# Optimization experiments

Hardware: AMD Instinct MI355X
Metric: run time of the kernel (lower is better)

## Reference

```python
import jax, jax.numpy as jnp
import numpy as np

NHEAD = 8
EPS = 1e-5


def ln(x, g, b):
    m = x.mean(-1, keepdims=True)
    v = ((x - m) ** 2).mean(-1, keepdims=True)
    return (x - m) * jax.lax.rsqrt(v + EPS) * g + b


def mha_rel(q_in, kv_in, pos_enc, pos_idx, Wqkv, bqkv, Wo, bo):
    # q_in, kv_in: [W, N, C] where N = hn*bs
    w, n, c = q_in.shape
    hd = c // NHEAD
    Wq, Wk, Wv = Wqkv[:c], Wqkv[c:2 * c], Wqkv[2 * c:]
    bq, bk, bv = bqkv[:c], bqkv[c:2 * c], bqkv[2 * c:]
    q = q_in @ Wq.T + bq
    k = kv_in @ Wk.T + bk
    v = kv_in @ Wv.T + bv
    # relative position lookup: [2W-1,1,C] gathered by flat [W*W] -> [W,W,C]
    pe = pos_enc[pos_idx].reshape(w, w, c)
    q_r = pe @ Wq.T + bq
    k_r = pe @ Wk.T + bk
    scale = hd ** -0.5
    q = (q * scale).reshape(w, n, NHEAD, hd)
    q_r = (q_r * scale).reshape(w, w, NHEAD, hd)
    k = k.reshape(w, n, NHEAD, hd)
    v = v.reshape(w, n, NHEAD, hd)
    k_r = k_r.reshape(w, w, NHEAD, hd)
    # content-content + content-pos + pos-content scores: [N, E, W, W']
    attn = (jnp.einsum('wnec,vnec->newv', q, k)
            + jnp.einsum('wnec,wvec->newv', q, k_r)
            + jnp.einsum('vnec,wvec->newv', k, q_r))
    raw = attn
    a = jax.nn.softmax(attn, axis=-1)
    vo = jnp.einsum('newv,vnec->wnec', a, v).reshape(w, n, c)
    vo = vo @ Wo.T + bo
    return vo, raw.sum(axis=1)  # [W,N,C], [N,W,W]


def setup_inputs() -> dict:
    key = jax.random.key(0)
    bs, c, hn, w = 2, 128, 64, 256
    ks = jax.random.split(key, 5)
    feat_left = jax.random.normal(ks[0], (bs, c, hn, w), jnp.float32)
    feat_right = jax.random.normal(ks[1], (bs, c, hn, w), jnp.float32)
    pos = jax.random.normal(ks[2], (2 * w - 1, 1, c), jnp.float32)
    r = jnp.arange(w)
    pos_indexes = (r[:, None] - r[None, :] + w - 1).reshape(-1).astype(jnp.int32)
    Wqkv = jax.random.normal(ks[3], (3 * c, c), jnp.float32) * 0.02
    bqkv = jnp.zeros((3 * c,), jnp.float32)
    Wo = jax.random.normal(ks[4], (c, c), jnp.float32) * 0.02
    bo = jnp.zeros((c,), jnp.float32)
    g1 = jnp.ones((c,), jnp.float32)
    b1 = jnp.zeros((c,), jnp.float32)
    g2 = jnp.ones((c,), jnp.float32)
    b2 = jnp.zeros((c,), jnp.float32)
    return dict(feat_left=feat_left, feat_right=feat_right, pos=pos,
                pos_indexes=pos_indexes, Wqkv=Wqkv, bqkv=bqkv, Wo=Wo, bo=bo,
                g1=g1, b1=b1, g2=g2, b2=b2)


def reference(feat_left, feat_right, pos, pos_indexes, Wqkv, bqkv, Wo, bo, g1, b1, g2, b2):
    bs, c, hn, w = feat_left.shape

    def to_seq(f):  # [bs,c,hn,w] -> [w, hn*bs, c]
        return jnp.transpose(f, (1, 3, 2, 0)).reshape(c, w, hn * bs).transpose(1, 2, 0)

    fl = to_seq(feat_left)
    fr = to_seq(feat_right)
    fl2 = ln(fl, g1, b1)
    fr2 = ln(fr, g1, b1)
    # right attends to left with flipped relative pos enc
    upd_r, _ = mha_rel(fr2, fl2, jnp.flip(pos, axis=0), pos_indexes, Wqkv, bqkv, Wo, bo)
    fr = fr + upd_r
    # left attends to updated right (last_layer=False -> no causal mask)
    fr2 = ln(fr, g2, b2)
    upd_l, raw = mha_rel(fl2, fr2, pos, pos_indexes, Wqkv, bqkv, Wo, bo)
    fl = fl + upd_l
    raw_attn = raw.reshape(hn, bs, w, w).transpose(1, 0, 2, 3)  # [bs,hn,w,w]

    def from_seq(f):  # [w, hn*bs, c] -> [bs,c,hn,w]
        return f.reshape(w, hn, bs, c).transpose(2, 3, 1, 0)

    return from_seq(fl), from_seq(fr), raw_attn
```

## Files before the change

### kernel.cpp

```cpp
#include <hip/hip_runtime.h>
#include <cstddef>

static constexpr int Wd  = 256;
static constexpr int NBd = 128;
static constexpr int Cd  = 128;
static constexpr int BSd = 2;
static constexpr int HNd = 64;
static constexpr size_t SEQF = (size_t)Wd * NBd * Cd;

typedef __attribute__((ext_vector_type(8))) short bf16x8;
typedef __attribute__((ext_vector_type(4))) short bf16x4;
typedef __attribute__((ext_vector_type(4))) float f32x4;
typedef __attribute__((ext_vector_type(2))) float f32x2;

__device__ inline short f2bf(float f) {
  union { float f; unsigned u; } v; v.f = f;
  return (short)((v.u + 0x7FFFu + ((v.u >> 16) & 1u)) >> 16);
}

__global__ __launch_bounds__(256) void k_to_seq_ln(
    const float* __restrict__ fA, const float* __restrict__ fB,
    float* __restrict__ seqA, float* __restrict__ seqB,
    short* __restrict__ lnA, short* __restrict__ lnB,
    const float* __restrict__ g, const float* __restrict__ bb) {
  __shared__ float red[2][8][33];
  __shared__ float mv[2][32];
  const int z = blockIdx.y;
  const float* feat = (z < 128) ? fA : fB;
  float* seq = (z < 128) ? seqA : seqB;
  short* lno = (z < 128) ? lnA : lnB;
  const int hb = z & 127;
  const int h = hb >> 1, b = hb & 1;
  const int n = h * BSd + b;
  const int w0 = blockIdx.x * 32;
  const int t = threadIdx.x;
  const int wl = t & 31, cg = t >> 5, c0 = cg * 16;
  float v[16];
  float s1 = 0.f, s2 = 0.f;
#pragma unroll
  for (int r = 0; r < 16; ++r) {
    v[r] = feat[(((size_t)b * Cd + c0 + r) * HNd + h) * Wd + w0 + wl];
    s1 += v[r]; s2 += v[r] * v[r];
  }
  red[0][cg][wl] = s1; red[1][cg][wl] = s2;
  __syncthreads();
  if (t < 32) {
    float a1 = 0.f, a2 = 0.f;
#pragma unroll
    for (int k = 0; k < 8; ++k) { a1 += red[0][k][t]; a2 += red[1][k][t]; }
    float mean = a1 * (1.0f / Cd);
    float var = a2 * (1.0f / Cd) - mean * mean;
    mv[0][t] = mean; mv[1][t] = rsqrtf(var + 1e-5f);
  }
  __syncthreads();
  const float mean = mv[0][wl], rstd = mv[1][wl];
  float* so = &seq[((size_t)(w0 + wl) * NBd + n) * Cd + c0];
  short* bo_ = &lno[((size_t)(w0 + wl) * NBd + n) * Cd + c0];
#pragma unroll
  for (int r = 0; r < 16; ++r) so[r] = v[r];
#pragma unroll
  for (int r = 0; r < 16; ++r)
    bo_[r] = f2bf((v[r] - mean) * rstd * g[c0 + r] + bb[c0 + r]);
}

__global__ __launch_bounds__(256) void k_from_seq2(const float* __restrict__ seqA,
                                                   const float* __restrict__ seqB,
                                                   float* __restrict__ featA,
                                                   float* __restrict__ featB) {
  __shared__ float tile[32][33];
  int wi0 = blockIdx.x * 32, ci0 = blockIdx.y * 32;
  int z = blockIdx.z;
  const float* seq = (z < 128) ? seqA : seqB;
  float* feat = (z < 128) ? featA : featB;
  int hb = z & 127;
  int h = hb >> 1, b = hb & 1;
  int n = h * BSd + b;
  int tx = threadIdx.x, ty = threadIdx.y;
#pragma unroll
  for (int r = 0; r < 4; ++r) {
    int wi = wi0 + ty + r * 8;
    tile[ty + r * 8][tx] = seq[((size_t)wi * NBd + n) * Cd + ci0 + tx];
  }
  __syncthreads();
#pragma unroll
  for (int r = 0; r < 4; ++r) {
    int ci = ci0 + ty + r * 8;
    feat[(((size_t)b * Cd + ci) * HNd + h) * Wd + wi0 + tx] = tile[tx][ty + r * 8];
  }
}

__global__ __launch_bounds__(256) void k_cvt(const float* __restrict__ w1, short* d1,
                                             const float* __restrict__ w2, short* d2,
                                             const float* __restrict__ w3, short* d3)
{
  int i = blockIdx.x * 256 + threadIdx.x;
  if (i < 49152) d1[i] = f2bf(w1[i]);
  if (i < 16384) d2[i] = f2bf(w2[i]);
  if (i < 65408) d3[i] = f2bf(w3[i]);
}

__global__ __launch_bounds__(256) void k_gemm_bf(
    const short* __restrict__ A, const short* __restrict__ Wt,
    const float* __restrict__ bias, float* __restrict__ outF,
    short* __restrict__ outB, int M, int ldout, int scaleN0, float scale,
    const short* __restrict__ A2, short* __restrict__ outB2, int ldout2, int yCut) {
  const int t = threadIdx.x;
  const int lane = t & 63, wv = t >> 6;
  const int ml = lane & 15, quad = lane >> 4;
  const int m0 = blockIdx.x * 64;
  int yb = blockIdx.y;
  const short* Ap = A;
  short* oB = outB;
  float* oF = outF;
  int ld = ldout;
  int nblk = yb;
  if (yb >= yCut) { Ap = A2; oB = outB2; oF = nullptr; ld = ldout2; nblk = 0; }
  const int n0 = nblk * 128 + wv * 32;
  const bf16x8 zero8 = {0, 0, 0, 0, 0, 0, 0, 0};

  bf16x8 Bfr[2][4];
#pragma unroll
  for (int nf = 0; nf < 2; ++nf)
#pragma unroll
    for (int ks = 0; ks < 4; ++ks)
      Bfr[nf][ks] = *(const bf16x8*)&Wt[(size_t)(n0 + nf * 16 + ml) * 128 + ks * 32 + quad * 8];

  f32x4 acc[4][2];
#pragma unroll
  for (int mf = 0; mf < 4; ++mf)
#pragma unroll
    for (int nf = 0; nf < 2; ++nf) acc[mf][nf] = {0.f, 0.f, 0.f, 0.f};

#pragma unroll
  for (int ks = 0; ks < 4; ++ks) {
    bf16x8 Af[4];
#pragma unroll
    for (int mf = 0; mf < 4; ++mf) {
      int m = m0 + mf * 16 + ml;
      Af[mf] = (m < M) ? *(const bf16x8*)&Ap[(size_t)m * 128 + ks * 32 + quad * 8] : zero8;
    }
#pragma unroll
    for (int mf = 0; mf < 4; ++mf)
#pragma unroll
      for (int nf = 0; nf < 2; ++nf)
        acc[mf][nf] = __builtin_amdgcn_mfma_f32_16x16x32_bf16(Af[mf], Bfr[nf][ks], acc[mf][nf], 0, 0, 0);
  }

#pragma unroll
  for (int nf = 0; nf < 2; ++nf) {
    int n = n0 + nf * 16 + ml;
    float bi = bias[n];
    float sc = (n < scaleN0) ? scale : 1.0f;
#pragma unroll
    for (int mf = 0; mf < 4; ++mf) {
#pragma unroll
      for (int r = 0; r < 4; ++r) {
        int m = m0 + mf * 16 + quad * 4 + r;
        if (m >= M) continue;
        float v = (acc[mf][nf][r] + bi) * sc;
        if (oF) oF[(size_t)m * ld + n] = v;
        if (oB) oB[(size_t)m * ld + n] = f2bf(v);
      }
    }
  }
}

__global__ __launch_bounds__(256) void k_gemm_wo_ln(
    const short* __restrict__ A, const short* __restrict__ Wt,
    const float* __restrict__ bias, const float* __restrict__ res,
    float* __restrict__ outF, short* __restrict__ outLN,
    const float* __restrict__ lng, const float* __restrict__ lnb) {
  const int t = threadIdx.x;
  const int lane = t & 63, wv = t >> 6;
  const int ml = lane & 15, quad = lane >> 4;
  const int m0 = blockIdx.x * 64 + wv * 16;
  const int ii = m0 >> 7;
  const int nn = (m0 & 127) + ml;

  f32x4 acc[8];
#pragma unroll
  for (int nf = 0; nf < 8; ++nf) acc[nf] = {0.f, 0.f, 0.f, 0.f};
#pragma unroll
  for (int ks = 0; ks < 4; ++ks) {
    bf16x8 Af = *(const bf16x8*)&A[(((size_t)nn * 8 + ks * 2 + (quad >> 1)) * 256 + ii) * 16 +
                                   (quad & 1) * 8];
#pragma unroll
    for (int nf = 0; nf < 8; ++nf) {
      bf16x8 Bf = *(const bf16x8*)&Wt[(size_t)(nf * 16 + ml) * 128 + ks * 32 + quad * 8];
      acc[nf] = __builtin_amdgcn_mfma_f32_16x16x32_bf16(Af, Bf, acc[nf], 0, 0, 0);
    }
  }
  float val[8][4];
#pragma unroll
  for (int nf = 0; nf < 8; ++nf) {
    float bi = bias[nf * 16 + ml];
#pragma unroll
    for (int r = 0; r < 4; ++r) {
      int m = m0 + quad * 4 + r;
      val[nf][r] = acc[nf][r] + bi + res[(size_t)m * 128 + nf * 16 + ml];
      outF[(size_t)m * 128 + nf * 16 + ml] = val[nf][r];
    }
  }
  if (outLN) {
#pragma unroll
    for (int r = 0; r < 4; ++r) {
      float s1 = 0.f, s2 = 0.f;
#pragma unroll
      for (int nf = 0; nf < 8; ++nf) { s1 += val[nf][r]; s2 += val[nf][r] * val[nf][r]; }
#pragma unroll
      for (int mk = 1; mk < 16; mk <<= 1) { s1 += __shfl_xor(s1, mk); s2 += __shfl_xor(s2, mk); }
      float mean = s1 * (1.0f / 128.f);
      float var = s2 * (1.0f / 128.f) - mean * mean;
      float rstd = rsqrtf(var + 1e-5f);
      int m = m0 + quad * 4 + r;
#pragma unroll
      for (int nf = 0; nf < 8; ++nf) {
        int nn2 = nf * 16 + ml;
        outLN[(size_t)m * 128 + nn2] = f2bf((val[nf][r] - mean) * rstd * lng[nn2] + lnb[nn2]);
      }
    }
  }
}

template <int PASS>
__global__ __launch_bounds__(256, 4) void k_attn_mfma(
    const short* __restrict__ Qg, int ldq,
    const short* __restrict__ Kg, const short* __restrict__ Vg, int ldkv,
    const short* __restrict__ PP, short* __restrict__ OT) {
  __shared__ short Ks[256][16];
  __shared__ short VTs[16][264];
  __shared__ float R2T[4][2][16][20];
  __shared__ float R3T[4][32][22];

  const int t = threadIdx.x;
  const int n = blockIdx.x;
  const int e = blockIdx.y;
  const int lane = t & 63, wv = t >> 6;
  const int ml = lane & 15, quad = lane >> 4;
  const bool lo = lane < 32;
  const bf16x8 zero8 = {0, 0, 0, 0, 0, 0, 0, 0};
  const f32x4 z4 = {0.f, 0.f, 0.f, 0.f};

#pragma unroll
  for (int it = 0; it < 4; ++it) {
    int idx = t + it * 256;
    int r = idx >> 2, c4 = idx & 3;
    *(bf16x4*)&Ks[r][c4 * 4] =
        *(const bf16x4*)&Kg[((size_t)r * NBd + n) * ldkv + e * 16 + c4 * 4];
  }
#pragma unroll
  for (int it = 0; it < 4; ++it) {
    bf16x4 vv = *(const bf16x4*)&Vg[((size_t)t * NBd + n) * ldkv + e * 16 + it * 4];
    VTs[it * 4 + 0][t] = vv[0];
    VTs[it * 4 + 1][t] = vv[1];
    VTs[it * 4 + 2][t] = vv[2];
    VTs[it * 4 + 3][t] = vv[3];
  }
  __syncthreads();

  const short* PPe = PP + e * 16;
  short* OTb = OT + (size_t)(n * 8 + e) * 256 * 16;

  for (int ip = 0; ip < 4; ++ip) {
    const int i0p = ip * 64;
    const int wb = (PASS == 2) ? i0p : (192 - i0p);
    bf16x8 bQ = lo ? *(const bf16x8*)&Qg[((size_t)(i0p + 16 * wv + ml) * NBd + n) * ldq +
                                         e * 16 + quad * 8]
                   : zero8;
    f32x4 Ot = {0.f, 0.f, 0.f, 0.f};
    float den = 0.f;

    bf16x8 fPQprev;
    {
      int pp = (PASS == 2) ? (wb + 16 * wv + 256 + ml) : (wb - 16 * wv + 48 + ml);
      if (pp > 510) pp = 510;
      const short* pr = &PPe[(size_t)pp * 256];
      bf16x8 fPK0 = lo ? *(const bf16x8*)&pr[128 + quad * 8] : zero8;
      fPQprev     = lo ? *(const bf16x8*)&pr[quad * 8] : zero8;
      f32x4 R2i = __builtin_amdgcn_mfma_f32_16x16x32_bf16(bQ, fPK0, z4, 0, 0, 0);
      *(f32x4*)&R2T[wv][1][ml][quad * 4] = R2i;
    }
    bf16x8 fPK, fPQf;
    {
      int pf = (PASS == 2) ? (wb + 16 * wv + 240 + ml) : (wb - 16 * wv + 64 + ml);
      if (pf > 510) pf = 510;
      const short* prf = &PPe[(size_t)pf * 256];
      fPK  = lo ? *(const bf16x8*)&prf[128 + quad * 8] : zero8;
      fPQf = lo ? *(const bf16x8*)&prf[quad * 8] : zero8;
    }

    unsigned pA0 = 0, pA1 = 0;
#pragma unroll
    for (int jt = 0; jt < 16; ++jt) {
      const int j0 = jt * 16;
      bf16x8 aK = lo ? *(const bf16x8*)&Ks[j0 + ml][quad * 8] : zero8;

      bf16x8 nPK = zero8, nPQ = zero8;
      if (jt < 15) {
        int pf = (PASS == 2) ? (wb + 16 * wv - (j0 + 16) + 240 + ml)
                             : (wb - 16 * wv + (j0 + 16) + 64 + ml);
        if (pf > 510) pf = 510;
        const short* prf = &PPe[(size_t)pf * 256];
        nPK = lo ? *(const bf16x8*)&prf[128 + quad * 8] : zero8;
        nPQ = lo ? *(const bf16x8*)&prf[quad * 8] : zero8;
      }

      f32x4 St  = __builtin_amdgcn_mfma_f32_16x16x32_bf16(aK, bQ, z4, 0, 0, 0);
      f32x4 R2f = __builtin_amdgcn_mfma_f32_16x16x32_bf16(bQ, fPK, z4, 0, 0, 0);
      f32x4 R3a_, R3b_;
      if (PASS == 2) {
        R3a_ = __builtin_amdgcn_mfma_f32_16x16x32_bf16(aK, fPQf, z4, 0, 0, 0);
        R3b_ = __builtin_amdgcn_mfma_f32_16x16x32_bf16(aK, fPQprev, z4, 0, 0, 0);
      } else {
        R3b_ = __builtin_amdgcn_mfma_f32_16x16x32_bf16(aK, fPQf, z4, 0, 0, 0);
        R3a_ = __builtin_amdgcn_mfma_f32_16x16x32_bf16(aK, fPQprev, z4, 0, 0, 0);
      }
      fPQprev = fPQf;
      fPK = nPK;
      fPQf = nPQ;

      *(f32x4*)&R2T[wv][jt & 1][ml][quad * 4] = R2f;
      *(f32x2*)&R3T[wv][ml][quad * 4]          = (f32x2){R3a_[0], R3a_[1]};
      *(f32x2*)&R3T[wv][ml][quad * 4 + 2]      = (f32x2){R3a_[2], R3a_[3]};
      *(f32x2*)&R3T[wv][ml + 16][quad * 4]     = (f32x2){R3b_[0], R3b_[1]};
      *(f32x2*)&R3T[wv][ml + 16][quad * 4 + 2] = (f32x2){R3b_[2], R3b_[3]};

      float pe4[4];
#pragma unroll
      for (int r = 0; r < 4; ++r) {
        const int jl = quad * 4 + r;
        const int pcol = (PASS == 2) ? (ml - jl + 15) : (jl - ml + 15);
        const int hi = pcol >> 4, col = pcol & 15;
        const int bk = (jt & 1) ^ hi ^ (PASS == 1 ? 1 : 0);
        float s = St[r] + R2T[wv][bk][col][ml] + R3T[wv][pcol][jl];
        pe4[r] = __expf(s);
        den += pe4[r];
      }
      unsigned d0, d1;
      asm("v_cvt_pk_bf16_f32 %0, %1, %2" : "=v"(d0) : "v"(pe4[0]), "v"(pe4[1]));
      asm("v_cvt_pk_bf16_f32 %0, %1, %2" : "=v"(d1) : "v"(pe4[2]), "v"(pe4[3]));
      if ((jt & 1) == 0) {
        pA0 = d0;
        pA1 = d1;
      } else {
        unsigned b0 = pA0, b2 = d0, b1 = pA1, b3 = d1;
        asm("v_permlane32_swap_b32 %0, %1" : "+v"(b0), "+v"(b2));
        asm("v_permlane16_swap_b32 %0, %1" : "+v"(b0), "+v"(b2));
        asm("v_permlane32_swap_b32 %0, %1" : "+v"(b1), "+v"(b3));
        asm("v_permlane16_swap_b32 %0, %1" : "+v"(b1), "+v"(b3));
        union { unsigned u[4]; bf16x8 v8; } bp;
        bp.u[0] = b0; bp.u[1] = b1; bp.u[2] = b2; bp.u[3] = b3;
        bf16x8 aVT = *(const bf16x8*)&VTs[ml][(jt >> 1) * 32 + quad * 8];
        Ot = __builtin_amdgcn_mfma_f32_16x16x32_bf16(aVT, bp.v8, Ot, 0, 0, 0);
      }
    }
    den += __shfl_xor(den, 16);
    den += __shfl_xor(den, 32);
    float inv = 1.f / den;
    bf16x4 ob;
    ob[0] = f2bf(Ot[0] * inv); ob[1] = f2bf(Ot[1] * inv);
    ob[2] = f2bf(Ot[2] * inv); ob[3] = f2bf(Ot[3] * inv);
    *(bf16x4*)&OTb[(size_t)(i0p + 16 * wv + ml) * 16 + quad * 4] = ob;
  }
}

__global__ __launch_bounds__(256, 4) void k_raw(
    const short* __restrict__ Qf, const short* __restrict__ Kf,
    const short* __restrict__ PP, float* __restrict__ raw) {
  __shared__ float R2s[4][2][16][17];
  __shared__ float R3s[4][16][34];
  const int t = threadIdx.x;
  const int n = blockIdx.y;
  const int lane = t & 63, wv = t >> 6;
  const int ml = lane & 15, quad = lane >> 4;
  const int it0 = blockIdx.x * 64 + wv * 16;
  const int jt0 = blockIdx.z * 4;
  const f32x4 z4 = {0.f, 0.f, 0.f, 0.f};

  bf16x8 aQ[4];
#pragma unroll
  for (int kc = 0; kc < 4; ++kc)
    aQ[kc] = *(const bf16x8*)&Qf[((size_t)(it0 + ml) * NBd + n) * 384 + kc * 32 + quad * 8];

  float* rbase = &raw[(((size_t)(n & 1) * HNd + (n >> 1)) * Wd + it0) * Wd];

  bf16x8 fPQprev[4];
  {
    int pp = it0 - jt0 * 16 + 256 + ml;
    if (pp > 510) pp = 510;
    const short* pr = &PP[(size_t)pp * 256];
    f32x4 R2i = z4;
#pragma unroll
    for (int kc = 0; kc < 4; ++kc) {
      bf16x8 fPK = *(const bf16x8*)&pr[128 + kc * 32 + quad * 8];
      R2i = __builtin_amdgcn_mfma_f32_16x16x32_bf16(aQ[kc], fPK, R2i, 0, 0, 0);
      fPQprev[kc] = *(const bf16x8*)&pr[kc * 32 + quad * 8];
    }
#pragma unroll
    for (int r = 0; r < 4; ++r) R2s[wv][1][quad * 4 + r][ml] = R2i[r];
  }

#pragma unroll
  for (int jq = 0; jq < 4; ++jq) {
    const int j0 = (jt0 + jq) * 16;
    bf16x8 aK[4];
#pragma unroll
    for (int kc = 0; kc < 4; ++kc)
      aK[kc] = *(const bf16x8*)&Kf[((size_t)(j0 + ml) * NBd + n) * 256 + kc * 32 + quad * 8];
    const int p0 = it0 - j0 + 240 + ml;
    const short* pr0 = &PP[(size_t)p0 * 256];
    f32x4 St = z4, R2f = z4, R3a = z4, R3b = z4;
    bf16x8 fPQ0[4];
#pragma unroll
    for (int kc = 0; kc < 4; ++kc)
      St = __builtin_amdgcn_mfma_f32_16x16x32_bf16(aQ[kc], aK[kc], St, 0, 0, 0);
#pragma unroll
    for (int kc = 0; kc < 4; ++kc) {
      bf16x8 fPK0 = *(const bf16x8*)&pr0[128 + kc * 32 + quad * 8];
      R2f = __builtin_amdgcn_mfma_f32_16x16x32_bf16(aQ[kc], fPK0, R2f, 0, 0, 0);
    }
#pragma unroll
    for (int kc = 0; kc < 4; ++kc) {
      fPQ0[kc] = *(const bf16x8*)&pr0[kc * 32 + quad * 8];
      R3a = __builtin_amdgcn_mfma_f32_16x16x32_bf16(aK[kc], fPQ0[kc], R3a, 0, 0, 0);
    }
#pragma unroll
    for (int kc = 0; kc < 4; ++kc)
      R3b = __builtin_amdgcn_mfma_f32_16x16x32_bf16(aK[kc], fPQprev[kc], R3b, 0, 0, 0);
#pragma unroll
    for (int kc = 0; kc < 4; ++kc) fPQprev[kc] = fPQ0[kc];
#pragma unroll
    for (int r = 0; r < 4; ++r) {
      R2s[wv][jq & 1][quad * 4 + r][ml] = R2f[r];
      R3s[wv][quad * 4 + r][ml]      = R3a[r];
      R3s[wv][quad * 4 + r][ml + 16] = R3b[r];
    }
#pragma unroll
    for (int r = 0; r < 4; ++r) {
      const int il = quad * 4 + r;
      const int pcol = il - ml + 15;
      const int hi = pcol >> 4, col = pcol & 15;
      const int bk = (jq & 1) ^ hi;
      rbase[(size_t)il * Wd + j0 + ml] = St[r] + R2s[wv][bk][il][col] + R3s[wv][ml][pcol];
    }
  }
}

extern "C" void kernel_launch(void* const* d_in, const int* in_sizes, int n_in,
                              void* d_out, int out_size, void* d_ws, size_t ws_size,
                              hipStream_t stream) {
  const float* feat_l = (const float*)d_in[0];
  const float* feat_r = (const float*)d_in[1];
  const float* pos    = (const float*)d_in[2];
  const float* Wqkv = (const float*)d_in[4];
  const float* bqkv = (const float*)d_in[5];
  const float* Wo   = (const float*)d_in[6];
  const float* bo   = (const float*)d_in[7];
  const float* g1   = (const float*)d_in[8];
  const float* b1   = (const float*)d_in[9];
  const float* g2   = (const float*)d_in[10];
  const float* b2   = (const float*)d_in[11];
  float* out = (float*)d_out;

  float* ws = (float*)d_ws;
  float* fl_seq = ws;
  float* fr_seq = ws + SEQF;
  float* fr2_f  = ws + 2 * SEQF;
  float* fl_new = ws + 3 * SEQF;
  short* wsb    = (short*)(ws + 4 * SEQF);
  short* fl2_b   = wsb;
  short* fr2_b   = wsb + SEQF;
  short* frb2_b  = wsb + 2 * SEQF;
  short* QKVl_b  = wsb + 3 * SEQF;
  short* Qr_b    = wsb + 6 * SEQF;
  short* KVr2_b  = wsb + 7 * SEQF;
  short* O_b     = wsb + 9 * SEQF;
  short* PP_b    = wsb + 10 * SEQF;
  short* Wb      = PP_b + 131072;
  short* pos_b   = Wb + 65536;

  k_to_seq_ln<<<dim3(8, 256), 256, 0, stream>>>(feat_l, feat_r, fl_seq, fr_seq,
                                                fl2_b, fr2_b, g1, b1);
  k_cvt<<<256, 256, 0, stream>>>(Wqkv, Wb, Wo, Wb + 49152, pos, pos_b);

  k_gemm_bf<<<dim3(8, 2), 256, 0, stream>>>(pos_b, Wb, bqkv, nullptr, PP_b,
                                            511, 256, 128, 0.25f,
                                            nullptr, nullptr, 0, 999);
  k_gemm_bf<<<dim3(512, 4), 256, 0, stream>>>(fl2_b, Wb, bqkv, nullptr, QKVl_b,
                                              32768, 384, 128, 0.25f,
                                              fr2_b, Qr_b, 128, 3);

  k_attn_mfma<1><<<dim3(128, 8), 256, 0, stream>>>(
      Qr_b, Cd, QKVl_b + 128, QKVl_b + 256, 384, PP_b, O_b);
  k_gemm_wo_ln<<<512, 256, 0, stream>>>(O_b, Wb + 49152, bo, fr_seq, fr2_f,
                                        frb2_b, g2, b2);
  k_gemm_bf<<<dim3(512, 2), 256, 0, stream>>>(frb2_b, Wb + 16384, bqkv + 128, nullptr,
                                              KVr2_b, 32768, 256, 0, 1.0f,
                                              nullptr, nullptr, 0, 999);
  k_attn_mfma<2><<<dim3(128, 8), 256, 0, stream>>>(
      QKVl_b, 384, KVr2_b, KVr2_b + 128, 256, PP_b, O_b);
  k_raw<<<dim3(4, 128, 4), 256, 0, stream>>>(QKVl_b, KVr2_b, PP_b, out + 2 * SEQF);
  k_gemm_wo_ln<<<512, 256, 0, stream>>>(O_b, Wb + 49152, bo, fl_seq, fl_new,
                                        nullptr, nullptr, nullptr);

  k_from_seq2<<<dim3(8, 4, 256), dim3(32, 8), 0, stream>>>(fl_new, fr2_f, out, out + SEQF);

  (void)in_sizes; (void)n_in; (void)out_size; (void)ws_size;
}
```

Baseline: 407.0 us.

## Software-pipeline attention tiles, replace R3 LDS transpose with bpermute, split query rows

The attention kernel is restructured so the MFMA work for key tile i is issued before the softmax consumption of tile i-1, overlapping matrix ops with the exp and accumulate work. The R3 shared-memory staging buffer is removed, and the needed diagonal values are gathered with ds_bpermute using lane addresses computed once per block. The grid gains a z dimension of 2 so each block handles half the query rows, doubling block count, and launch bounds are raised to 5 blocks per CU. The trade-off is higher register pressure from carrying the previous tile's results, plus K/V loads repeated by twice as many blocks.

```diff
diff --git a/kernel.cpp b/kernel.cpp
--- a/kernel.cpp
+++ b/kernel.cpp
@@ -223,14 +223,13 @@
 }
 
 template <int PASS>
-__global__ __launch_bounds__(256, 4) void k_attn_mfma(
+__global__ __launch_bounds__(256, 5) void k_attn_mfma(
     const short* __restrict__ Qg, int ldq,
     const short* __restrict__ Kg, const short* __restrict__ Vg, int ldkv,
     const short* __restrict__ PP, short* __restrict__ OT) {
   __shared__ short Ks[256][16];
   __shared__ short VTs[16][264];
   __shared__ float R2T[4][2][16][20];
-  __shared__ float R3T[4][32][22];
 
   const int t = threadIdx.x;
   const int n = blockIdx.x;
@@ -258,11 +257,21 @@
   }
   __syncthreads();
 
+  int bpa[4], hiR[4], colR[4];
+#pragma unroll
+  for (int r = 0; r < 4; ++r) {
+    int jl = quad * 4 + r;
+    int pcol = (PASS == 2) ? (ml - jl + 15) : (jl - ml + 15);
+    hiR[r] = pcol >> 4;
+    colR[r] = pcol & 15;
+    bpa[r] = ((pcol & 15) | (quad << 4)) << 2;
+  }
+
   const short* PPe = PP + e * 16;
   short* OTb = OT + (size_t)(n * 8 + e) * 256 * 16;
 
-  for (int ip = 0; ip < 4; ++ip) {
-    const int i0p = ip * 64;
+  for (int ipl = 0; ipl < 2; ++ipl) {
+    const int i0p = ((int)blockIdx.z * 2 + ipl) * 64;
     const int wb = (PASS == 2) ? i0p : (192 - i0p);
     bf16x8 bQ = lo ? *(const bf16x8*)&Qg[((size_t)(i0p + 16 * wv + ml) * NBd + n) * ldq +
                                          e * 16 + quad * 8]
@@ -289,57 +298,49 @@
       fPQf = lo ? *(const bf16x8*)&prf[quad * 8] : zero8;
     }
 
+    f32x4 St_p, R3a_p, R3b_p;
     unsigned pA0 = 0, pA1 = 0;
-#pragma unroll
-    for (int jt = 0; jt < 16; ++jt) {
-      const int j0 = jt * 16;
-      bf16x8 aK = lo ? *(const bf16x8*)&Ks[j0 + ml][quad * 8] : zero8;
-
-      bf16x8 nPK = zero8, nPQ = zero8;
-      if (jt < 15) {
-        int pf = (PASS == 2) ? (wb + 16 * wv - (j0 + 16) + 240 + ml)
-                             : (wb - 16 * wv + (j0 + 16) + 64 + ml);
+
+    {
+      bf16x8 aK = lo ? *(const bf16x8*)&Ks[ml][quad * 8] : zero8;
+      St_p = __builtin_amdgcn_mfma_f32_16x16x32_bf16(aK, bQ, z4, 0, 0, 0);
+      f32x4 R2c = __builtin_amdgcn_mfma_f32_16x16x32_bf16(bQ, fPK, z4, 0, 0, 0);
+      if (PASS == 2) {
+        R3a_p = __builtin_amdgcn_mfma_f32_16x16x32_bf16(aK, fPQf, z4, 0, 0, 0);
+        R3b_p = __builtin_amdgcn_mfma_f32_16x16x32_bf16(aK, fPQprev, z4, 0, 0, 0);
+      } else {
+        R3b_p = __builtin_amdgcn_mfma_f32_16x16x32_bf16(aK, fPQf, z4, 0, 0, 0);
+        R3a_p = __builtin_amdgcn_mfma_f32_16x16x32_bf16(aK, fPQprev, z4, 0, 0, 0);
+      }
+      fPQprev = fPQf;
+      {
+        int pf = (PASS == 2) ? (wb + 16 * wv - 16 + 240 + ml) : (wb - 16 * wv + 16 + 64 + ml);
         if (pf > 510) pf = 510;
         const short* prf = &PPe[(size_t)pf * 256];
-        nPK = lo ? *(const bf16x8*)&prf[128 + quad * 8] : zero8;
-        nPQ = lo ? *(const bf16x8*)&prf[quad * 8] : zero8;
-      }
-
-      f32x4 St  = __builtin_amdgcn_mfma_f32_16x16x32_bf16(aK, bQ, z4, 0, 0, 0);
-      f32x4 R2f = __builtin_amdgcn_mfma_f32_16x16x32_bf16(bQ, fPK, z4, 0, 0, 0);
-      f32x4 R3a_, R3b_;
-      if (PASS == 2) {
-        R3a_ = __builtin_amdgcn_mfma_f32_16x16x32_bf16(aK, fPQf, z4, 0, 0, 0);
-        R3b_ = __builtin_amdgcn_mfma_f32_16x16x32_bf16(aK, fPQprev, z4, 0, 0, 0);
-      } else {
-        R3b_ = __builtin_amdgcn_mfma_f32_16x16x32_bf16(aK, fPQf, z4, 0, 0, 0);
-        R3a_ = __builtin_amdgcn_mfma_f32_16x16x32_bf16(aK, fPQprev, z4, 0, 0, 0);
-      }
-      fPQprev = fPQf;
-      fPK = nPK;
-      fPQf = nPQ;
-
-      *(f32x4*)&R2T[wv][jt & 1][ml][quad * 4] = R2f;
-      *(f32x2*)&R3T[wv][ml][quad * 4]          = (f32x2){R3a_[0], R3a_[1]};
-      *(f32x2*)&R3T[wv][ml][quad * 4 + 2]      = (f32x2){R3a_[2], R3a_[3]};
-      *(f32x2*)&R3T[wv][ml + 16][quad * 4]     = (f32x2){R3b_[0], R3b_[1]};
-      *(f32x2*)&R3T[wv][ml + 16][quad * 4 + 2] = (f32x2){R3b_[2], R3b_[3]};
-
+        fPK  = lo ? *(const bf16x8*)&prf[128 + quad * 8] : zero8;
+        fPQf = lo ? *(const bf16x8*)&prf[quad * 8] : zero8;
+      }
+      *(f32x4*)&R2T[wv][0][ml][quad * 4] = R2c;
+    }
+
+    auto consume = [&](int T) {
       float pe4[4];
 #pragma unroll
       for (int r = 0; r < 4; ++r) {
-        const int jl = quad * 4 + r;
-        const int pcol = (PASS == 2) ? (ml - jl + 15) : (jl - ml + 15);
-        const int hi = pcol >> 4, col = pcol & 15;
-        const int bk = (jt & 1) ^ hi ^ (PASS == 1 ? 1 : 0);
-        float s = St[r] + R2T[wv][bk][col][ml] + R3T[wv][pcol][jl];
+        int bk = (T & 1) ^ hiR[r] ^ (PASS == 1 ? 1 : 0);
+        float r2 = R2T[wv][bk][colR[r]][ml];
+        float va = __int_as_float(
+            __builtin_amdgcn_ds_bpermute(bpa[r], __float_as_int(R3a_p[r])));
+        float vb = __int_as_float(
+            __builtin_amdgcn_ds_bpermute(bpa[r], __float_as_int(R3b_p[r])));
+        float s = St_p[r] + r2 + (hiR[r] ? vb : va);
         pe4[r] = __expf(s);
         den += pe4[r];
       }
       unsigned d0, d1;
       asm("v_cvt_pk_bf16_f32 %0, %1, %2" : "=v"(d0) : "v"(pe4[0]), "v"(pe4[1]));
       asm("v_cvt_pk_bf16_f32 %0, %1, %2" : "=v"(d1) : "v"(pe4[2]), "v"(pe4[3]));
-      if ((jt & 1) == 0) {
+      if ((T & 1) == 0) {
         pA0 = d0;
         pA1 = d1;
       } else {
@@ -350,10 +351,40 @@
         asm("v_permlane16_swap_b32 %0, %1" : "+v"(b1), "+v"(b3));
         union { unsigned u[4]; bf16x8 v8; } bp;
         bp.u[0] = b0; bp.u[1] = b1; bp.u[2] = b2; bp.u[3] = b3;
-        bf16x8 aVT = *(const bf16x8*)&VTs[ml][(jt >> 1) * 32 + quad * 8];
+        bf16x8 aVT = *(const bf16x8*)&VTs[ml][(T >> 1) * 32 + quad * 8];
         Ot = __builtin_amdgcn_mfma_f32_16x16x32_bf16(aVT, bp.v8, Ot, 0, 0, 0);
       }
-    }
+    };
+
+#pragma unroll
+    for (int i = 1; i < 16; ++i) {
+      const int j0 = i * 16;
+      bf16x8 aK = lo ? *(const bf16x8*)&Ks[j0 + ml][quad * 8] : zero8;
+      f32x4 St_c = __builtin_amdgcn_mfma_f32_16x16x32_bf16(aK, bQ, z4, 0, 0, 0);
+      f32x4 R2c  = __builtin_amdgcn_mfma_f32_16x16x32_bf16(bQ, fPK, z4, 0, 0, 0);
+      f32x4 R3A, R3B;
+      if (PASS == 2) {
+        R3A = __builtin_amdgcn_mfma_f32_16x16x32_bf16(aK, fPQf, z4, 0, 0, 0);
+        R3B = __builtin_amdgcn_mfma_f32_16x16x32_bf16(aK, fPQprev, z4, 0, 0, 0);
+      } else {
+        R3B = __builtin_amdgcn_mfma_f32_16x16x32_bf16(aK, fPQf, z4, 0, 0, 0);
+        R3A = __builtin_amdgcn_mfma_f32_16x16x32_bf16(aK, fPQprev, z4, 0, 0, 0);
+      }
+      fPQprev = fPQf;
+      if (i < 15) {
+        int pf = (PASS == 2) ? (wb + 16 * wv - (j0 + 16) + 240 + ml)
+                             : (wb - 16 * wv + (j0 + 16) + 64 + ml);
+        if (pf > 510) pf = 510;
+        const short* prf = &PPe[(size_t)pf * 256];
+        fPK  = lo ? *(const bf16x8*)&prf[128 + quad * 8] : zero8;
+        fPQf = lo ? *(const bf16x8*)&prf[quad * 8] : zero8;
+      }
+      consume(i - 1);
+      *(f32x4*)&R2T[wv][i & 1][ml][quad * 4] = R2c;
+      St_p = St_c; R3a_p = R3A; R3b_p = R3B;
+    }
+    consume(15);
+
     den += __shfl_xor(den, 16);
     den += __shfl_xor(den, 32);
     float inv = 1.f / den;
@@ -490,14 +521,14 @@
                                               32768, 384, 128, 0.25f,
                                               fr2_b, Qr_b, 128, 3);
 
-  k_attn_mfma<1><<<dim3(128, 8), 256, 0, stream>>>(
+  k_attn_mfma<1><<<dim3(128, 8, 2), 256, 0, stream>>>(
       Qr_b, Cd, QKVl_b + 128, QKVl_b + 256, 384, PP_b, O_b);
   k_gemm_wo_ln<<<512, 256, 0, stream>>>(O_b, Wb + 49152, bo, fr_seq, fr2_f,
                                         frb2_b, g2, b2);
   k_gemm_bf<<<dim3(512, 2), 256, 0, stream>>>(frb2_b, Wb + 16384, bqkv + 128, nullptr,
                                               KVr2_b, 32768, 256, 0, 1.0f,
                                               nullptr, nullptr, 0, 999);
-  k_attn_mfma<2><<<dim3(128, 8), 256, 0, stream>>>(
+  k_attn_mfma<2><<<dim3(128, 8, 2), 256, 0, stream>>>(
       QKVl_b, 384, KVr2_b, KVr2_b + 128, 256, PP_b, O_b);
   k_raw<<<dim3(4, 128, 4), 256, 0, stream>>>(QKVl_b, KVr2_b, PP_b, out + 2 * SEQF);
   k_gemm_wo_ln<<<512, 256, 0, stream>>>(O_b, Wb + 49152, bo, fl_seq, fl_new,
```

After: 492.2 us. +20.9%, slower.
